# Kernel optimization log

Measured on AMD Instinct MI355X. Metric: run time of the kernel, lower is better.

The kernel has to match this reference:

```python
import jax, jax.numpy as jnp
import numpy as np

B, T, C = 4, 2048, 1024

def setup_inputs() -> dict:
    key = jax.random.key(0)
    kx, kq, kk, kv = jax.random.split(key, 4)
    s = C ** -0.5  # match nn.Linear init scale roughly
    return {
        "x": jax.random.normal(kx, (B, T, C), dtype=jnp.float32),
        "Wq": jax.random.normal(kq, (C, C), dtype=jnp.float32) * s,
        "Wk": jax.random.normal(kk, (C, C), dtype=jnp.float32) * s,
        "Wv": jax.random.normal(kv, (C, C), dtype=jnp.float32) * s,
    }

def reference(x, Wq, Wk, Wv):
    Bq, Tq, Cq = x.shape
    # nn.Linear: y = x @ W^T (bias=False)
    q = jnp.einsum('btc,dc->btd', x, Wq)
    k = jnp.einsum('btc,dc->btd', x, Wk)
    v = jnp.einsum('btc,dc->btd', x, Wv)
    scale = Cq ** -0.5
    qk = jnp.einsum('btd,bsd->bts', q, k) * scale  # [B, T, T]
    causal = jnp.tril(jnp.ones((Tq, Tq), dtype=bool))
    qk = jnp.where(causal, qk, -jnp.inf)
    attn = jax.nn.softmax(qk, axis=-1)
    out = jnp.einsum('bts,bsd->btd', attn, v)
    return out
```

## Files before the change

### kernel.cpp

```cpp
#include <hip/hip_runtime.h>
#include <hip/hip_fp16.h>


typedef __attribute__((ext_vector_type(8))) _Float16 half8;
typedef __attribute__((ext_vector_type(4))) _Float16 half4;
typedef __attribute__((ext_vector_type(4))) float f32x4;

template<int TM, int TN, int WM, int WN, bool SWAP>
__device__ __forceinline__ void gemm_nt_core(
    const _Float16* __restrict__ A, const _Float16* __restrict__ B,
    int lda, int ldb, int k0, int k1,
    _Float16* ldsA, _Float16* ldsB,
    f32x4 acc[TM / (WM * 16)][TN / (WN * 16)])
{
    constexpr int FM = TM / (WM * 16), FN = TN / (WN * 16);
    constexpr int NA = TM / 32, NB = TN / 32;
    const int t    = threadIdx.x;
    const int lane = t & 63;
    const int w    = t >> 6;
    const int wm   = w % WM;
    const int wn   = w / WM;
    const int lr   = lane & 15;
    const int lq   = lane >> 4;

    const _Float16* ga[NA]; int loA[NA];
    const _Float16* gb[NB]; int loB[NB];
#pragma unroll
    for (int i = 0; i < NA; ++i) {
        int f = t + 256 * i;
        int r = f >> 3, c = (f & 7) ^ ((f >> 3) & 7);
        ga[i] = A + (size_t)r * lda + c * 8;
        loA[i] = f * 8;
    }
#pragma unroll
    for (int i = 0; i < NB; ++i) {
        int f = t + 256 * i;
        int r = f >> 3, c = (f & 7) ^ ((f >> 3) & 7);
        gb[i] = B + (size_t)r * ldb + c * 8;
        loB[i] = f * 8;
    }

    int offA[2][FM], offB[2][FN];
#pragma unroll
    for (int h = 0; h < 2; ++h) {
#pragma unroll
        for (int i = 0; i < FM; ++i) {
            int R = wm * (TM / WM) + i * 16 + lr;
            offA[h][i] = (8 * R + ((h * 4 + lq) ^ (R & 7))) * 8;
        }
#pragma unroll
        for (int i = 0; i < FN; ++i) {
            int R = wn * (TN / WN) + i * 16 + lr;
            offB[h][i] = (8 * R + ((h * 4 + lq) ^ (R & 7))) * 8;
        }
    }

    half8 va[NA], vb[NB];
#pragma unroll
    for (int i = 0; i < NA; ++i) va[i] = *(const half8*)(ga[i] + k0);
#pragma unroll
    for (int i = 0; i < NB; ++i) vb[i] = *(const half8*)(gb[i] + k0);

    for (int k = k0; k < k1; k += 64) {
        __syncthreads();
#pragma unroll
        for (int i = 0; i < NA; ++i) *(half8*)(ldsA + loA[i]) = va[i];
#pragma unroll
        for (int i = 0; i < NB; ++i) *(half8*)(ldsB + loB[i]) = vb[i];
        if (k + 64 < k1) {
#pragma unroll
            for (int i = 0; i < NA; ++i) va[i] = *(const half8*)(ga[i] + k + 64);
#pragma unroll
            for (int i = 0; i < NB; ++i) vb[i] = *(const half8*)(gb[i] + k + 64);
        }
        __syncthreads();

#pragma unroll
        for (int h = 0; h < 2; ++h) {
            half8 af[FM], bf[FN];
#pragma unroll
            for (int i = 0; i < FM; ++i) af[i] = *(const half8*)(ldsA + offA[h][i]);
#pragma unroll
            for (int i = 0; i < FN; ++i) bf[i] = *(const half8*)(ldsB + offB[h][i]);
#pragma unroll
            for (int mi = 0; mi < FM; ++mi)
#pragma unroll
                for (int ni = 0; ni < FN; ++ni) {
                    if constexpr (SWAP)
                        acc[mi][ni] = __builtin_amdgcn_mfma_f32_16x16x32_f16(
                            bf[ni], af[mi], acc[mi][ni], 0, 0, 0);
                    else
                        acc[mi][ni] = __builtin_amdgcn_mfma_f32_16x16x32_f16(
                            af[mi], bf[ni], acc[mi][ni], 0, 0, 0);
                }
        }
    }
}

__device__ __forceinline__ void gload_lds16(const void* g, void* l)
{
    __builtin_amdgcn_global_load_lds(
        (const __attribute__((address_space(1))) void*)g,
        (__attribute__((address_space(3))) void*)l, 16, 0, 0);
}

template<bool SWAP>
__device__ __forceinline__ void gemm_nt_256x128(
    const _Float16* __restrict__ A, const _Float16* __restrict__ B,
    const int lda, const int ldb, const int kTiles,
    _Float16* lds, f32x4 acc[4][4])
{
    const int t    = threadIdx.x;
    const int lane = t & 63;
    const int w    = t >> 6;
    const int wm   = w & 3;
    const int wn   = w >> 2;
    const int lr   = lane & 15;
    const int lq   = lane >> 4;

    const int r0 = t >> 3;
    const int c0 = (t & 7) ^ (r0 & 7);
    const _Float16* gA = A + (size_t)r0 * lda + c0 * 8;
    const _Float16* gB = B + (size_t)r0 * ldb + c0 * 8;

    char* ldsc = (char*)lds;
    char* stA = ldsc + w * 1024;
    char* stB = ldsc + 65536 + w * 1024;

    const int x0 = ((0 + lq) ^ (lr & 7)) * 16;
    const int x1 = ((4 + lq) ^ (lr & 7)) * 16;
    const char* rdA = ldsc + wm * 8192 + lr * 128;
    const char* rdB = ldsc + 65536 + wn * 8192 + lr * 128;

    half8 af[4][2], bf01[2][2], bf23[2][2];

#define STGA1(BUF, S, KOFF)                                                   \
    gload_lds16(gA + (size_t)(S) * 64 * lda + (KOFF),                         \
                stA + (BUF) * 32768 + (S) * 8192)

#define STGB1(BUF, S, KOFF)                                                   \
    gload_lds16(gB + (size_t)(S) * 64 * ldb + (KOFF),                         \
                stB + (BUF) * 16384 + (S) * 8192)

#define LDA_ALL(BUF) do {                                                     \
    const char* _p = rdA + (BUF) * 32768;                                     \
    _Pragma("unroll")                                                         \
    for (int mi = 0; mi < 4; ++mi) {                                          \
        af[mi][0] = *(const half8*)(_p + mi * 2048 + x0);                     \
        af[mi][1] = *(const half8*)(_p + mi * 2048 + x1);                     \
    }                                                                         \
} while (0)

#define LDB_H(DST, BUF, NQ) do {                                              \
    const char* _p = rdB + (BUF) * 16384 + (NQ) * 4096;                       \
    _Pragma("unroll")                                                         \
    for (int ni = 0; ni < 2; ++ni) {                                          \
        DST[ni][0] = *(const half8*)(_p + ni * 2048 + x0);                    \
        DST[ni][1] = *(const half8*)(_p + ni * 2048 + x1);                    \
    }                                                                         \
} while (0)

#define MFMA_NH(NQ, BSRC) do {                                                \
    _Pragma("unroll")                                                         \
    for (int mi = 0; mi < 4; ++mi)                                            \
    _Pragma("unroll")                                                         \
    for (int ni = 0; ni < 2; ++ni)                                            \
    _Pragma("unroll")                                                         \
    for (int kh = 0; kh < 2; ++kh) {                                          \
        if constexpr (SWAP)                                                   \
            acc[mi][(NQ)*2+ni] = __builtin_amdgcn_mfma_f32_16x16x32_f16(      \
                BSRC[ni][kh], af[mi][kh], acc[mi][(NQ)*2+ni], 0, 0, 0);       \
        else                                                                  \
            acc[mi][(NQ)*2+ni] = __builtin_amdgcn_mfma_f32_16x16x32_f16(      \
                af[mi][kh], BSRC[ni][kh], acc[mi][(NQ)*2+ni], 0, 0, 0);       \
    }                                                                         \
} while (0)

#define PH_PRE() do {                                                         \
    asm volatile("" ::: "memory");                                            \
    __builtin_amdgcn_s_barrier();                                             \
    asm volatile("s_waitcnt lgkmcnt(0)" ::: "memory");                        \
    __builtin_amdgcn_sched_barrier(0);                                        \
    __builtin_amdgcn_s_setprio(1);                                            \
} while (0)

#define PH_POST() do {                                                        \
    __builtin_amdgcn_s_setprio(0);                                            \
    __builtin_amdgcn_sched_barrier(0);                                        \
    __builtin_amdgcn_s_barrier();                                             \
    asm volatile("" ::: "memory");                                            \
} while (0)

#define KTILE(KT, BUF) do {                                                   \
    const int _k1 = ((KT) + 1) * 64, _k2 = ((KT) + 2) * 64;                   \
    const bool _s1 = (KT) + 1 < kTiles, _s2 = (KT) + 2 < kTiles;              \
                                                                     \
    LDA_ALL(BUF);                                                             \
    LDB_H(bf01, BUF, 0);                                                      \
    if (_s1) { STGB1((BUF) ^ 1, 0, _k1); STGB1((BUF) ^ 1, 1, _k1); }          \
    PH_PRE(); MFMA_NH(0, bf01); PH_POST();                                    \
                                                                     \
    LDB_H(bf23, BUF, 1);                                                      \
    if (_s2) { STGA1(BUF, 0, _k2); STGA1(BUF, 1, _k2);                        \
               STGA1(BUF, 2, _k2); STGA1(BUF, 3, _k2); }                      \
    asm volatile("" ::: "memory");                                            \
    __builtin_amdgcn_s_barrier();                                             \
    asm volatile("s_waitcnt lgkmcnt(0)" ::: "memory");                        \
    __builtin_amdgcn_sched_barrier(0);                                        \
    __builtin_amdgcn_s_setprio(1);                                            \
    MFMA_NH(1, bf23);                                                         \
    __builtin_amdgcn_s_setprio(0);                                            \
    if (_s2) asm volatile("s_waitcnt vmcnt(4)" ::: "memory");                 \
    else     asm volatile("s_waitcnt vmcnt(0)" ::: "memory");                 \
    __builtin_amdgcn_sched_barrier(0);                                        \
    __builtin_amdgcn_s_barrier();                                             \
    asm volatile("" ::: "memory");                                            \
} while (0)

    STGA1(0, 0, 0); STGA1(0, 1, 0); STGA1(0, 2, 0); STGA1(0, 3, 0);
    STGB1(0, 0, 0); STGB1(0, 1, 0);
    if (kTiles > 1) { STGA1(1, 0, 64); STGA1(1, 1, 64);
                      STGA1(1, 2, 64); STGA1(1, 3, 64); }
    if (kTiles > 1) asm volatile("s_waitcnt vmcnt(4)" ::: "memory");
    else            asm volatile("s_waitcnt vmcnt(0)" ::: "memory");
    __builtin_amdgcn_sched_barrier(0);
    __builtin_amdgcn_s_barrier();
    asm volatile("" ::: "memory");

#pragma unroll 1
    for (int kt = 0; kt < kTiles; kt += 2) {
        KTILE(kt, 0);
        KTILE(kt + 1, 1);
    }

#undef STGA1
#undef STGB1
#undef LDA_ALL
#undef LDB_H
#undef MFMA_NH
#undef PH_PRE
#undef PH_POST
#undef KTILE
}

__global__ __launch_bounds__(256) void convert_k(
    const float* __restrict__ x, const float* __restrict__ Wq,
    const float* __restrict__ Wk, const float* __restrict__ Wv,
    _Float16* __restrict__ xh, _Float16* __restrict__ Wh,
    float* __restrict__ rsum)
{
    int g = blockIdx.x * 256 + threadIdx.x;
    if (g < 2048) {
        f32x4 z = { 0.f, 0.f, 0.f, 0.f };
        *(f32x4*)(rsum + g * 4) = z;
    }
    int i = g * 4;
    const float* src;
    _Float16* dst;
    if (i < 8388608) {
        src = x + i; dst = xh + i;
    } else {
        int j = i - 8388608;
        int wsel = j >> 20;
        int off  = j & 1048575;
        src = (wsel == 0 ? Wq : wsel == 1 ? Wk : Wv) + off;
        dst = Wh + j;
    }
    float4 f = *(const float4*)src;
    half4 h = { (_Float16)f.x, (_Float16)f.y, (_Float16)f.z, (_Float16)f.w };
    *(half4*)dst = h;
}

__global__ __launch_bounds__(512, 2) void qkv_gemm256_k(
    const _Float16* __restrict__ xh, const _Float16* __restrict__ Wh,
    _Float16* __restrict__ Q, _Float16* __restrict__ K,
    _Float16* __restrict__ Vt)
{
    __shared__ __align__(16) _Float16 lds[49152];
    const int tileM = blockIdx.x * 256;
    const int tileN = blockIdx.y * 128;
    const int z     = blockIdx.z;
    const _Float16* W = Wh + (size_t)z * 1024 * 1024;

    const int lane = threadIdx.x & 63;
    const int w    = threadIdx.x >> 6;
    const int wm = w & 3, wn = w >> 2;
    const int lr = lane & 15, lq = lane >> 4;

    f32x4 acc[4][4] = {};
    if (z == 2) {
        gemm_nt_256x128<false>(xh + (size_t)tileM * 1024,
                               W + (size_t)tileN * 1024,
                               1024, 1024, 16, lds, acc);
#pragma unroll
        for (int mi = 0; mi < 4; ++mi)
#pragma unroll
            for (int ni = 0; ni < 4; ++ni) {
                int m0 = tileM + wm * 64 + mi * 16 + lq * 4;
                int n  = tileN + wn * 64 + ni * 16 + lr;
                int b = m0 >> 11, tt = m0 & 2047;
                half4 h = { (_Float16)acc[mi][ni][0], (_Float16)acc[mi][ni][1],
                            (_Float16)acc[mi][ni][2], (_Float16)acc[mi][ni][3] };
                *(half4*)(Vt + (size_t)b * 2048 * 1024 + (size_t)n * 2048 + tt) = h;
            }
    } else {
        gemm_nt_256x128<true>(xh + (size_t)tileM * 1024,
                              W + (size_t)tileN * 1024,
                              1024, 1024, 16, lds, acc);
        _Float16* O = (z == 0) ? Q : K;
#pragma unroll
        for (int mi = 0; mi < 4; ++mi)
#pragma unroll
            for (int ni = 0; ni < 4; ++ni) {
                int tt = tileM + wm * 64 + mi * 16 + lr;
                int d0 = tileN + wn * 64 + ni * 16 + lq * 4;
                half4 h = { (_Float16)acc[mi][ni][0], (_Float16)acc[mi][ni][1],
                            (_Float16)acc[mi][ni][2], (_Float16)acc[mi][ni][3] };
                *(half4*)(O + (size_t)tt * 1024 + d0) = h;
            }
    }
}

__global__ __launch_bounds__(256) void scores_gemm_k(
    const _Float16* __restrict__ Q, const _Float16* __restrict__ K,
    _Float16* __restrict__ S, float* __restrict__ rsum)
{
    const int bid = blockIdx.x;
    const int n   = (bid & 7) * 68 + (bid >> 3);
    const int b   = n / 136;
    const int m   = n - b * 136;
    int ti = (int)((sqrtf(8.f * (float)m + 1.f) - 1.f) * 0.5f);
    while ((ti + 1) * (ti + 2) / 2 <= m) ++ti;
    while (ti * (ti + 1) / 2 > m) --ti;
    const int si = m - ti * (ti + 1) / 2;
    const int tileT = ti * 128, tileS = si * 128;

    __shared__ __align__(16) _Float16 ldsA[128 * 64];
    __shared__ __align__(16) _Float16 ldsB[128 * 64];
    f32x4 acc[4][4] = {};
    gemm_nt_core<128, 128, 2, 2, true>(
        Q + (size_t)b * 2048 * 1024 + (size_t)tileT * 1024,
        K + (size_t)b * 2048 * 1024 + (size_t)tileS * 1024,
        1024, 1024, 0, 1024, ldsA, ldsB, acc);

    const int lane = threadIdx.x & 63;
    const int w    = threadIdx.x >> 6;
    const int wm = w & 1, wn = w >> 1;
    const int lr = lane & 15, lq = lane >> 4;
    const float scale = 0.03125f;

    float rp[4] = { 0.f, 0.f, 0.f, 0.f };
#pragma unroll
    for (int mi = 0; mi < 4; ++mi)
#pragma unroll
        for (int ni = 0; ni < 4; ++ni) {
            int tt = tileT + wm * 64 + mi * 16 + lr;
            int s0 = tileS + wn * 64 + ni * 16 + lq * 4;
            half4 h;
#pragma unroll
            for (int r = 0; r < 4; ++r) {
                float e = __expf(fmaf(acc[mi][ni][r], scale, -6.0f));
                h[r] = (s0 + r <= tt) ? (_Float16)e : (_Float16)0.f;
                rp[mi] += (float)h[r];
            }
            *(half4*)(S + ((size_t)b * 2048 + tt) * 2048 + s0) = h;
        }

#pragma unroll
    for (int mi = 0; mi < 4; ++mi) {
        rp[mi] += __shfl_xor(rp[mi], 16);
        rp[mi] += __shfl_xor(rp[mi], 32);
    }
    if (lq == 0) {
#pragma unroll
        for (int mi = 0; mi < 4; ++mi) {
            int tt = tileT + wm * 64 + mi * 16 + lr;
            atomicAdd(&rsum[(size_t)b * 2048 + tt], rp[mi]);
        }
    }
}

__global__ __launch_bounds__(256) void pv_gemm_k(
    const _Float16* __restrict__ P, const _Float16* __restrict__ Vt,
    const float* __restrict__ rsum, float* __restrict__ out)
{
    __shared__ __align__(16) _Float16 ldsA[128 * 64];
    __shared__ __align__(16) _Float16 ldsB[128 * 64];
    const int tileT = (15 - blockIdx.x) * 128;
    const int tileD = blockIdx.y * 128;
    const int b     = blockIdx.z;
    const int kEnd  = tileT + 128;

    f32x4 acc[4][4] = {};
    gemm_nt_core<128, 128, 2, 2, true>(
        P + ((size_t)b * 2048 + tileT) * 2048,
        Vt + (size_t)b * 1024 * 2048 + (size_t)tileD * 2048,
        2048, 2048, 0, kEnd, ldsA, ldsB, acc);

    const int lane = threadIdx.x & 63;
    const int w    = threadIdx.x >> 6;
    const int wm = w & 1, wn = w >> 1;
    const int lr = lane & 15, lq = lane >> 4;

#pragma unroll
    for (int mi = 0; mi < 4; ++mi) {
        const int tt = tileT + wm * 64 + mi * 16 + lr;
        const float inv = 1.0f / rsum[(size_t)b * 2048 + tt];
#pragma unroll
        for (int ni = 0; ni < 4; ++ni) {
            int d0 = tileD + wn * 64 + ni * 16 + lq * 4;
            f32x4 o = { acc[mi][ni][0] * inv, acc[mi][ni][1] * inv,
                        acc[mi][ni][2] * inv, acc[mi][ni][3] * inv };
            *(f32x4*)(out + ((size_t)b * 2048 + tt) * 1024 + d0) = o;
        }
    }
}

extern "C" void kernel_launch(void* const* d_in, const int* in_sizes, int n_in,
                              void* d_out, int out_size, void* d_ws, size_t ws_size,
                              hipStream_t stream)
{
    const float* x  = (const float*)d_in[0];
    const float* Wq = (const float*)d_in[1];
    const float* Wk = (const float*)d_in[2];
    const float* Wv = (const float*)d_in[3];
    float* out = (float*)d_out;

    char* ws = (char*)d_ws;
    _Float16* xh = (_Float16*)(ws);
    _Float16* Wh = (_Float16*)(ws + (16u << 20));
    _Float16* Qh = (_Float16*)(ws + (22u << 20));
    _Float16* Kh = (_Float16*)(ws + (38u << 20));
    _Float16* Vt = (_Float16*)(ws + (54u << 20));
    _Float16* S  = (_Float16*)(ws + (70u << 20));
    float*    rs = (float*)   (ws + (102u << 20));

    convert_k<<<11264, 256, 0, stream>>>(x, Wq, Wk, Wv, xh, Wh, rs);

    qkv_gemm256_k<<<dim3(32, 8, 3), 512, 0, stream>>>(xh, Wh, Qh, Kh, Vt);

    scores_gemm_k<<<544, 256, 0, stream>>>(Qh, Kh, S, rs);
    pv_gemm_k<<<dim3(16, 8, 4), 256, 0, stream>>>(S, Vt, rs, out);
}
```

Measured before the change: 235.4 us.

## Fuse scores and PV kernels via a persistent grid-wide barrier

Merges the scores GEMM and PV GEMM into a single launch. All 544 blocks first compute their score tiles, then meet at a global atomic-counter barrier that convert_k resets, and 512 of them go on to compute the PV tiles. The aim is to remove one kernel launch and the tail gap between the two phases. It depends on all 544 blocks being co-resident (launch bounds of 3 per CU on a 256-CU part), otherwise the spin barrier deadlocks, and it adds spin time on the barrier.

```diff
diff --git a/kernel.cpp b/kernel.cpp
--- a/kernel.cpp
+++ b/kernel.cpp
@@ -254,6 +254,7 @@
         f32x4 z = { 0.f, 0.f, 0.f, 0.f };
         *(f32x4*)(rsum + g * 4) = z;
     }
+    if (g == 2048) *(unsigned*)(rsum + 8192) = 0u;
     int i = g * 4;
     const float* src;
     _Float16* dst;
@@ -321,97 +322,108 @@
     }
 }
 
-__global__ __launch_bounds__(256) void scores_gemm_k(
+__global__ __launch_bounds__(256, 3) void attn_sp_k(
     const _Float16* __restrict__ Q, const _Float16* __restrict__ K,
-    _Float16* __restrict__ S, float* __restrict__ rsum)
-{
-    const int bid = blockIdx.x;
-    const int n   = (bid & 7) * 68 + (bid >> 3);
-    const int b   = n / 136;
-    const int m   = n - b * 136;
-    int ti = (int)((sqrtf(8.f * (float)m + 1.f) - 1.f) * 0.5f);
-    while ((ti + 1) * (ti + 2) / 2 <= m) ++ti;
-    while (ti * (ti + 1) / 2 > m) --ti;
-    const int si = m - ti * (ti + 1) / 2;
-    const int tileT = ti * 128, tileS = si * 128;
-
+    _Float16* S, const _Float16* __restrict__ Vt,
+    float* rsum, unsigned* bar, float* __restrict__ out)
+{
     __shared__ __align__(16) _Float16 ldsA[128 * 64];
     __shared__ __align__(16) _Float16 ldsB[128 * 64];
-    f32x4 acc[4][4] = {};
-    gemm_nt_core<128, 128, 2, 2, true>(
-        Q + (size_t)b * 2048 * 1024 + (size_t)tileT * 1024,
-        K + (size_t)b * 2048 * 1024 + (size_t)tileS * 1024,
-        1024, 1024, 0, 1024, ldsA, ldsB, acc);
 
     const int lane = threadIdx.x & 63;
     const int w    = threadIdx.x >> 6;
     const int wm = w & 1, wn = w >> 1;
     const int lr = lane & 15, lq = lane >> 4;
-    const float scale = 0.03125f;
-
-    float rp[4] = { 0.f, 0.f, 0.f, 0.f };
-#pragma unroll
-    for (int mi = 0; mi < 4; ++mi)
-#pragma unroll
-        for (int ni = 0; ni < 4; ++ni) {
-            int tt = tileT + wm * 64 + mi * 16 + lr;
-            int s0 = tileS + wn * 64 + ni * 16 + lq * 4;
-            half4 h;
-#pragma unroll
-            for (int r = 0; r < 4; ++r) {
-                float e = __expf(fmaf(acc[mi][ni][r], scale, -6.0f));
-                h[r] = (s0 + r <= tt) ? (_Float16)e : (_Float16)0.f;
-                rp[mi] += (float)h[r];
+
+    {
+        const int bid = blockIdx.x;
+        const int n   = (bid & 7) * 68 + (bid >> 3);
+        const int b   = n / 136;
+        const int m   = n - b * 136;
+        int ti = (int)((sqrtf(8.f * (float)m + 1.f) - 1.f) * 0.5f);
+        while ((ti + 1) * (ti + 2) / 2 <= m) ++ti;
+        while (ti * (ti + 1) / 2 > m) --ti;
+        const int si = m - ti * (ti + 1) / 2;
+        const int tileT = ti * 128, tileS = si * 128;
+
+        f32x4 acc[4][4] = {};
+        gemm_nt_core<128, 128, 2, 2, true>(
+            Q + (size_t)b * 2048 * 1024 + (size_t)tileT * 1024,
+            K + (size_t)b * 2048 * 1024 + (size_t)tileS * 1024,
+            1024, 1024, 0, 1024, ldsA, ldsB, acc);
+
+        const float scale = 0.03125f;
+        float rp[4] = { 0.f, 0.f, 0.f, 0.f };
+#pragma unroll
+        for (int mi = 0; mi < 4; ++mi)
+#pragma unroll
+            for (int ni = 0; ni < 4; ++ni) {
+                int tt = tileT + wm * 64 + mi * 16 + lr;
+                int s0 = tileS + wn * 64 + ni * 16 + lq * 4;
+                half4 h;
+#pragma unroll
+                for (int r = 0; r < 4; ++r) {
+                    float e = __expf(fmaf(acc[mi][ni][r], scale, -6.0f));
+                    h[r] = (s0 + r <= tt) ? (_Float16)e : (_Float16)0.f;
+                    rp[mi] += (float)h[r];
+                }
+                *(half4*)(S + ((size_t)b * 2048 + tt) * 2048 + s0) = h;
             }
-            *(half4*)(S + ((size_t)b * 2048 + tt) * 2048 + s0) = h;
-        }
-
-#pragma unroll
-    for (int mi = 0; mi < 4; ++mi) {
-        rp[mi] += __shfl_xor(rp[mi], 16);
-        rp[mi] += __shfl_xor(rp[mi], 32);
-    }
-    if (lq == 0) {
+
 #pragma unroll
         for (int mi = 0; mi < 4; ++mi) {
-            int tt = tileT + wm * 64 + mi * 16 + lr;
-            atomicAdd(&rsum[(size_t)b * 2048 + tt], rp[mi]);
-        }
-    }
-}
-
-__global__ __launch_bounds__(256) void pv_gemm_k(
-    const _Float16* __restrict__ P, const _Float16* __restrict__ Vt,
-    const float* __restrict__ rsum, float* __restrict__ out)
-{
-    __shared__ __align__(16) _Float16 ldsA[128 * 64];
-    __shared__ __align__(16) _Float16 ldsB[128 * 64];
-    const int tileT = (15 - blockIdx.x) * 128;
-    const int tileD = blockIdx.y * 128;
-    const int b     = blockIdx.z;
-    const int kEnd  = tileT + 128;
-
-    f32x4 acc[4][4] = {};
-    gemm_nt_core<128, 128, 2, 2, true>(
-        P + ((size_t)b * 2048 + tileT) * 2048,
-        Vt + (size_t)b * 1024 * 2048 + (size_t)tileD * 2048,
-        2048, 2048, 0, kEnd, ldsA, ldsB, acc);
-
-    const int lane = threadIdx.x & 63;
-    const int w    = threadIdx.x >> 6;
-    const int wm = w & 1, wn = w >> 1;
-    const int lr = lane & 15, lq = lane >> 4;
-
-#pragma unroll
-    for (int mi = 0; mi < 4; ++mi) {
-        const int tt = tileT + wm * 64 + mi * 16 + lr;
-        const float inv = 1.0f / rsum[(size_t)b * 2048 + tt];
-#pragma unroll
-        for (int ni = 0; ni < 4; ++ni) {
-            int d0 = tileD + wn * 64 + ni * 16 + lq * 4;
-            f32x4 o = { acc[mi][ni][0] * inv, acc[mi][ni][1] * inv,
-                        acc[mi][ni][2] * inv, acc[mi][ni][3] * inv };
-            *(f32x4*)(out + ((size_t)b * 2048 + tt) * 1024 + d0) = o;
+            rp[mi] += __shfl_xor(rp[mi], 16);
+            rp[mi] += __shfl_xor(rp[mi], 32);
+        }
+        if (lq == 0) {
+#pragma unroll
+            for (int mi = 0; mi < 4; ++mi) {
+                int tt = tileT + wm * 64 + mi * 16 + lr;
+                atomicAdd(&rsum[(size_t)b * 2048 + tt], rp[mi]);
+            }
+        }
+    }
+
+    __syncthreads();
+    __threadfence();
+    if (threadIdx.x == 0) {
+        __hip_atomic_fetch_add(bar, 1u, __ATOMIC_ACQ_REL,
+                               __HIP_MEMORY_SCOPE_AGENT);
+        unsigned v;
+        do {
+            v = __hip_atomic_load(bar, __ATOMIC_ACQUIRE,
+                                  __HIP_MEMORY_SCOPE_AGENT);
+        } while (v < 544u);
+    }
+    __syncthreads();
+    __threadfence();
+
+    if (blockIdx.x < 512) {
+        const int n2 = blockIdx.x;
+        const int d  = n2 & 7;
+        const int tio = (n2 >> 3) & 15;
+        const int b   = n2 >> 7;
+        const int tileT = (15 - tio) * 128;
+        const int tileD = d * 128;
+        const int kEnd  = tileT + 128;
+
+        f32x4 acc[4][4] = {};
+        gemm_nt_core<128, 128, 2, 2, true>(
+            S + ((size_t)b * 2048 + tileT) * 2048,
+            Vt + (size_t)b * 1024 * 2048 + (size_t)tileD * 2048,
+            2048, 2048, 0, kEnd, ldsA, ldsB, acc);
+
+#pragma unroll
+        for (int mi = 0; mi < 4; ++mi) {
+            const int tt = tileT + wm * 64 + mi * 16 + lr;
+            const float inv = 1.0f / rsum[(size_t)b * 2048 + tt];
+#pragma unroll
+            for (int ni = 0; ni < 4; ++ni) {
+                int d0 = tileD + wn * 64 + ni * 16 + lq * 4;
+                f32x4 o = { acc[mi][ni][0] * inv, acc[mi][ni][1] * inv,
+                            acc[mi][ni][2] * inv, acc[mi][ni][3] * inv };
+                *(f32x4*)(out + ((size_t)b * 2048 + tt) * 1024 + d0) = o;
+            }
         }
     }
 }
@@ -434,11 +446,11 @@
     _Float16* Vt = (_Float16*)(ws + (54u << 20));
     _Float16* S  = (_Float16*)(ws + (70u << 20));
     float*    rs = (float*)   (ws + (102u << 20));
+    unsigned* bar = (unsigned*)(rs + 8192);
 
     convert_k<<<11264, 256, 0, stream>>>(x, Wq, Wk, Wv, xh, Wh, rs);
 
     qkv_gemm256_k<<<dim3(32, 8, 3), 512, 0, stream>>>(xh, Wh, Qh, Kh, Vt);
 
-    scores_gemm_k<<<544, 256, 0, stream>>>(Qh, Kh, S, rs);
-    pv_gemm_k<<<dim3(16, 8, 4), 256, 0, stream>>>(S, Vt, rs, out);
-}
+    attn_sp_k<<<544, 256, 0, stream>>>(Qh, Kh, S, Vt, rs, bar, out);
+}
```

Result: slower. 429.1 us (+82.3%).
